# Performance work log

Hardware: AMD Instinct MI355X
Metric: run time of the kernel (lower is better)

## Reference

```python
import jax, jax.numpy as jnp
import numpy as np

B, S, D_MODEL = 4, 2048, 1024
NUM_HEADS, HEAD_DIM = 16, 64
EPS = 1e-6


def setup_inputs() -> dict:
    key = jax.random.key(0)
    ks = jax.random.split(key, 6)
    hd = NUM_HEADS * HEAD_DIM
    scale_in = 1.0 / np.sqrt(D_MODEL)
    scale_hd = 1.0 / np.sqrt(hd)
    return {
        "x": jax.random.normal(ks[0], (B, S, D_MODEL), dtype=jnp.float32),
        "w_q": jax.random.normal(ks[1], (D_MODEL, hd), dtype=jnp.float32) * scale_in,
        "w_k": jax.random.normal(ks[2], (D_MODEL, hd), dtype=jnp.float32) * scale_in,
        "w_v": jax.random.normal(ks[3], (D_MODEL, hd), dtype=jnp.float32) * scale_in,
        "w_proj": jax.random.normal(ks[4], (hd, D_MODEL), dtype=jnp.float32) * scale_hd,
        "b_proj": jax.random.normal(ks[5], (D_MODEL,), dtype=jnp.float32) * 0.01,
        "ln_gamma": jnp.ones((D_MODEL,), dtype=jnp.float32),
        "ln_beta": jnp.zeros((D_MODEL,), dtype=jnp.float32),
    }


def reference(x, w_q, w_k, w_v, w_proj, b_proj, ln_gamma, ln_beta):
    # x: [B, S, D]; project and split heads -> [B, H, S, Dh]
    def split_heads(t):
        b, s, _ = t.shape
        return t.reshape(b, s, NUM_HEADS, HEAD_DIM).transpose(0, 2, 1, 3)

    q = split_heads(x @ w_q)
    k = split_heads(x @ w_k)
    v = split_heads(x @ w_v)

    scale = HEAD_DIM ** (-0.5)
    attn = jnp.einsum("bnqd,bnkd->bnqk", q, k) * scale  # [B, H, S, S]
    attn = jax.nn.softmax(attn, axis=-1)
    o = jnp.einsum("bnqk,bnkd->bnqd", attn, v)  # [B, H, S, Dh]
    o = o.transpose(0, 2, 1, 3).reshape(x.shape[0], x.shape[1], NUM_HEADS * HEAD_DIM)

    # proj + residual (dropout = identity in eval) then LayerNorm(eps=1e-6)
    y = o @ w_proj + b_proj + x
    mean = jnp.mean(y, axis=-1, keepdims=True)
    var = jnp.var(y, axis=-1, keepdims=True)
    y = (y - mean) * jax.lax.rsqrt(var + EPS) * ln_gamma + ln_beta
    return y
```

## Files before the change

kernel.cpp:

```cpp
#include <hip/hip_runtime.h>
#include <hip/hip_fp16.h>


typedef unsigned short u16;
typedef __attribute__((ext_vector_type(8))) u16 u16x8;
typedef __attribute__((ext_vector_type(4))) u16 u16x4;
typedef __attribute__((ext_vector_type(2))) unsigned int u32x2;
typedef __attribute__((ext_vector_type(8))) __bf16 bf16x8;
typedef __attribute__((ext_vector_type(8))) _Float16 f16x8;
typedef __attribute__((ext_vector_type(4))) _Float16 f16x4;
typedef __attribute__((ext_vector_type(2))) _Float16 f16x2;
typedef __attribute__((ext_vector_type(2))) __fp16 hf16x2;
typedef __attribute__((ext_vector_type(4))) float f32x4;

#define SM_C1 0.1803368801111204f

static __device__ __forceinline__ u16 f2bf(float f) {
  union { float f; unsigned int u; } v; v.f = f;
  unsigned int u = v.u;
  return (u16)((u + 0x7fffu + ((u >> 16) & 1u)) >> 16);
}
static __device__ __forceinline__ float bf2f(u16 b) {
  union { unsigned int u; float f; } v; v.u = ((unsigned int)b) << 16;
  return v.f;
}
static __device__ __forceinline__ u16 f2h(float f) {
  union { _Float16 h; u16 u; } v; v.h = (_Float16)f;
  return v.u;
}

static __device__ __forceinline__ void gld16(const u16* g, u16* l) {
  __builtin_amdgcn_global_load_lds((const __attribute__((address_space(1))) void*)g,
                                   (__attribute__((address_space(3))) void*)l, 16, 0, 0);
}


__global__ __launch_bounds__(256) void k_convx(const float* __restrict__ x,
                                               u16* __restrict__ xbf) {
  int i = (blockIdx.x * 256 + threadIdx.x) * 8;
  float4 a = *(const float4*)(x + i);
  float4 b = *(const float4*)(x + i + 4);
  u16x8 o;
  o[0] = f2bf(a.x); o[1] = f2bf(a.y); o[2] = f2bf(a.z); o[3] = f2bf(a.w);
  o[4] = f2bf(b.x); o[5] = f2bf(b.y); o[6] = f2bf(b.z); o[7] = f2bf(b.w);
  *(u16x8*)(xbf + i) = o;
}

__global__ __launch_bounds__(256) void k_convwT(const float* __restrict__ w0,
                                                const float* __restrict__ w1,
                                                const float* __restrict__ w2,
                                                const float* __restrict__ w3,
                                                u16* __restrict__ o0, u16* __restrict__ o1,
                                                u16* __restrict__ o2, u16* __restrict__ o3) {
  __shared__ float tile[64][65];
  const float* w = blockIdx.z == 0 ? w0 : blockIdx.z == 1 ? w1 : blockIdx.z == 2 ? w2 : w3;
  u16* o = blockIdx.z == 0 ? o0 : blockIdx.z == 1 ? o1 : blockIdx.z == 2 ? o2 : o3;
  const int k0 = blockIdx.x * 64, n0 = blockIdx.y * 64;
  const int t = threadIdx.x;
#pragma unroll
  for (int i = 0; i < 16; i++) {
    int idx = t + 256 * i;
    int k = idx >> 6, n = idx & 63;
    tile[k][n] = w[(k0 + k) * 1024 + n0 + n];
  }
  __syncthreads();
#pragma unroll
  for (int i = 0; i < 16; i++) {
    int idx = t + 256 * i;
    int n = idx >> 6, k = idx & 63;
    o[(n0 + n) * 1024 + k0 + k] = f2bf(tile[k][n]);
  }
}


__global__ __launch_bounds__(256) void k_gemm_qkv(const u16* __restrict__ xbf,
                                                  const u16* __restrict__ wT,
                                                  u16* __restrict__ Qb, u16* __restrict__ Kb,
                                                  u16* __restrict__ VbT) {
  __shared__ alignas(16) u16 Als[128 * 64];
  __shared__ alignas(16) u16 Bls[128 * 64];
  const int t = threadIdx.x;
  const int wv = t >> 6, lane = t & 63, quad = lane >> 4, l16 = lane & 15;
  const int wm = wv >> 1, wn = wv & 1;
  const int m0 = blockIdx.x * 128;
  const int nt = blockIdx.y;
  const int row = t >> 3;
  const int kg = (t & 7) ^ (row & 7);
  const u16* aG = xbf + (size_t)(m0 + row) * 1024 + kg * 8;
  const u16* bG = wT + (size_t)(nt * 128 + row) * 1024 + kg * 8;
  const int sw = l16 & 7;
  const int aA0 = (wm * 64 + l16) * 64 + ((quad) ^ sw) * 8;
  const int aA1 = (wm * 64 + l16) * 64 + ((4 + quad) ^ sw) * 8;
  const int bA0 = (wn * 64 + l16) * 64 + ((quad) ^ sw) * 8;
  const int bA1 = (wn * 64 + l16) * 64 + ((4 + quad) ^ sw) * 8;

  f32x4 acc[4][4] = {};
  for (int k0 = 0; k0 < 1024; k0 += 64) {
    __syncthreads();
#pragma unroll
    for (int i = 0; i < 4; i++) {
      gld16(aG + i * 32 * 1024 + k0, &Als[(i * 256 + wv * 64) * 8]);
      gld16(bG + i * 32 * 1024 + k0, &Bls[(i * 256 + wv * 64) * 8]);
    }
    __syncthreads();
#pragma unroll
    for (int c = 0; c < 2; c++) {
      bf16x8 a[4], b[4];
#pragma unroll
      for (int f = 0; f < 4; f++) a[f] = *(const bf16x8*)&Als[(c ? aA1 : aA0) + f * 1024];
#pragma unroll
      for (int g = 0; g < 4; g++) b[g] = *(const bf16x8*)&Bls[(c ? bA1 : bA0) + g * 1024];
#pragma unroll
      for (int f = 0; f < 4; f++)
#pragma unroll
        for (int g = 0; g < 4; g++)
          acc[f][g] = __builtin_amdgcn_mfma_f32_16x16x32_bf16(a[f], b[g], acc[f][g], 0, 0, 0);
    }
  }

  const int sel = nt >> 3;
  const int n0 = (nt & 7) * 128 + wn * 64;
  const int mBase = m0 + wm * 64 + quad * 4;
  if (sel < 2) {
    u16* Ob = sel == 0 ? Qb : Kb;
    const float scl = sel == 0 ? SM_C1 : 1.0f;
#pragma unroll
    for (int f = 0; f < 4; f++)
#pragma unroll
      for (int g = 0; g < 4; g++)
#pragma unroll
        for (int r = 0; r < 4; r++) {
          int m = mBase + f * 16 + r;
          int n = n0 + g * 16 + l16;
          Ob[(size_t)m * 1024 + n] = f2bf(acc[f][g][r] * scl);
        }
  } else {
#pragma unroll
    for (int f = 0; f < 4; f++) {
      int m = mBase + f * 16;
      int bb = m >> 11, s = m & 2047;
#pragma unroll
      for (int g = 0; g < 4; g++) {
        int n = n0 + g * 16 + l16;
        int hh = n >> 6, dh = n & 63;
        u16x4 o;
#pragma unroll
        for (int r = 0; r < 4; r++) o[r] = f2h(acc[f][g][r]);
        *(u16x4*)&VbT[(size_t)(((bb << 4) + hh) * 64 + dh) * 2048 + s] = o;
      }
    }
  }
}


__global__ __launch_bounds__(256) void k_gemm_proj(const u16* __restrict__ Abf,
                                                   const u16* __restrict__ wT,
                                                   const float* __restrict__ x,
                                                   const float* __restrict__ bias,
                                                   u16* __restrict__ ypre) {
  __shared__ alignas(16) u16 Als[128 * 64];
  __shared__ alignas(16) u16 Bls[128 * 64];
  const int t = threadIdx.x;
  const int wv = t >> 6, lane = t & 63, quad = lane >> 4, l16 = lane & 15;
  const int wm = wv >> 1, wn = wv & 1;
  const int m0 = blockIdx.x * 128;
  const int n0t = blockIdx.y * 128;
  const int row = t >> 3;
  const int kg = (t & 7) ^ (row & 7);
  const u16* aG = Abf + (size_t)(m0 + row) * 1024 + kg * 8;
  const u16* bG = wT + (size_t)(n0t + row) * 1024 + kg * 8;
  const int sw = l16 & 7;
  const int aA0 = (wm * 64 + l16) * 64 + ((quad) ^ sw) * 8;
  const int aA1 = (wm * 64 + l16) * 64 + ((4 + quad) ^ sw) * 8;
  const int bA0 = (wn * 64 + l16) * 64 + ((quad) ^ sw) * 8;
  const int bA1 = (wn * 64 + l16) * 64 + ((4 + quad) ^ sw) * 8;

  f32x4 acc[4][4] = {};
  for (int k0 = 0; k0 < 1024; k0 += 64) {
    __syncthreads();
#pragma unroll
    for (int i = 0; i < 4; i++) {
      gld16(aG + i * 32 * 1024 + k0, &Als[(i * 256 + wv * 64) * 8]);
      gld16(bG + i * 32 * 1024 + k0, &Bls[(i * 256 + wv * 64) * 8]);
    }
    __syncthreads();
#pragma unroll
    for (int c = 0; c < 2; c++) {
      bf16x8 a[4], b[4];
#pragma unroll
      for (int f = 0; f < 4; f++) a[f] = *(const bf16x8*)&Als[(c ? aA1 : aA0) + f * 1024];
#pragma unroll
      for (int g = 0; g < 4; g++) b[g] = *(const bf16x8*)&Bls[(c ? bA1 : bA0) + g * 1024];
#pragma unroll
      for (int f = 0; f < 4; f++)
#pragma unroll
        for (int g = 0; g < 4; g++)
          acc[f][g] = __builtin_amdgcn_mfma_f32_16x16x32_bf16(a[f], b[g], acc[f][g], 0, 0, 0);
    }
  }

  const int n0 = n0t + wn * 64;
  const int mBase = m0 + wm * 64 + quad * 4;
#pragma unroll
  for (int g = 0; g < 4; g++) {
    int n = n0 + g * 16 + l16;
    float bn = bias[n];
#pragma unroll
    for (int f = 0; f < 4; f++)
#pragma unroll
      for (int r = 0; r < 4; r++) {
        int m = mBase + f * 16 + r;
        ypre[(size_t)m * 1024 + n] = f2bf(acc[f][g][r] + bn + x[(size_t)m * 1024 + n]);
      }
  }
}


__global__ __launch_bounds__(256, 2) void k_attn(const u16* __restrict__ Qb,
                                                 const u16* __restrict__ Kb,
                                                 const u16* __restrict__ VbT,
                                                 u16* __restrict__ Ob) {
  __shared__ alignas(16) u16 smem[4][64 * 72];
  const int b = blockIdx.x >> 4, h = blockIdx.x & 15;
  const int q0 = blockIdx.y * 256;
  const int t = threadIdx.x;
  const int wave = t >> 6, lane = t & 63, quad = lane >> 4, l16 = lane & 15;
  const int sr = t >> 2, sc = (t & 3) * 8;

  bf16x8 aq[4][2];
#pragma unroll
  for (int qf = 0; qf < 4; qf++)
#pragma unroll
    for (int c = 0; c < 2; c++)
      aq[qf][c] = *(const bf16x8*)&Qb[(size_t)(b * 2048 + q0 + wave * 64 + qf * 16 + l16) * 1024 +
                                      h * 64 + c * 32 + quad * 8];

  f32x4 Oacc[4][4] = {};
  float psum[4] = {};

  const u16* kBase = Kb + (size_t)(b * 2048) * 1024 + h * 64;
  const u16* vtRow = VbT + (size_t)((b * 16 + h) * 64 + sr) * 2048;

  u16x8 rk0, rk1, rv0, rv1;
  {
    const u16* kR = kBase + (size_t)sr * 1024;
    rk0 = *(const u16x8*)(kR + sc);
    rk1 = *(const u16x8*)(kR + sc + 32);
    rv0 = *(const u16x8*)(vtRow + sc);
    rv1 = *(const u16x8*)(vtRow + sc + 32);
  }

  for (int kt = 0; kt < 32; kt++) {
    const int p = kt & 1;
    u16* Kls = smem[p];
    u16* Vls = smem[2 + p];
    *(u16x8*)&Kls[sr * 72 + sc]      = rk0;
    *(u16x8*)&Kls[sr * 72 + sc + 32] = rk1;
    *(u16x8*)&Vls[sr * 72 + sc]      = rv0;
    *(u16x8*)&Vls[sr * 72 + sc + 32] = rv1;
    __syncthreads();
    if (kt < 31) {
      const int kv1 = (kt + 1) * 64;
      const u16* kR = kBase + (size_t)(kv1 + sr) * 1024;
      rk0 = *(const u16x8*)(kR + sc);
      rk1 = *(const u16x8*)(kR + sc + 32);
      rv0 = *(const u16x8*)(vtRow + kv1 + sc);
      rv1 = *(const u16x8*)(vtRow + kv1 + sc + 32);
    }

    f32x4 st[4][4];
#pragma unroll
    for (int qf = 0; qf < 4; qf++)
#pragma unroll
      for (int f = 0; f < 4; f++) st[qf][f] = f32x4{0.f, 0.f, 0.f, 0.f};
#pragma unroll
    for (int c = 0; c < 2; c++) {
      bf16x8 bk[4];
#pragma unroll
      for (int f = 0; f < 4; f++)
        bk[f] = *(const bf16x8*)&Kls[(f * 16 + l16) * 72 + c * 32 + quad * 8];
#pragma unroll
      for (int qf = 0; qf < 4; qf++)
#pragma unroll
        for (int f = 0; f < 4; f++)
          st[qf][f] = __builtin_amdgcn_mfma_f32_16x16x32_bf16(bk[f], aq[qf][c], st[qf][f], 0, 0, 0);
    }

    f16x8 va[2][4];
#pragma unroll
    for (int kf = 0; kf < 2; kf++)
#pragma unroll
      for (int g = 0; g < 4; g++)
        va[kf][g] = *(const f16x8*)&Vls[(g * 16 + l16) * 72 + kf * 32 + quad * 8];

#pragma unroll
    for (int qf = 0; qf < 4; qf++) {
      union PK { hf16x2 r; f16x2 v; __half2 h; unsigned int u; };
      PK e01[4], e23[4];
      __half2 it2 = __half2{__half(0.f), __half(0.f)};
#pragma unroll
      for (int f = 0; f < 4; f++) {
        PK a01, a23;
        a01.r = __builtin_amdgcn_cvt_pkrtz(st[qf][f][0], st[qf][f][1]);
        a23.r = __builtin_amdgcn_cvt_pkrtz(st[qf][f][2], st[qf][f][3]);
        e01[f].h = h2exp2(a01.h);
        e23[f].h = h2exp2(a23.h);
        it2 = __hadd2(it2, __hadd2(e01[f].h, e23[f].h));
      }
      psum[qf] += __low2float(it2) + __high2float(it2);
#pragma unroll
      for (int kf = 0; kf < 2; kf++) {
        u32x2 sa = __builtin_amdgcn_permlane32_swap(e01[2 * kf].u, e01[2 * kf + 1].u, false, false);
        u32x2 sb = __builtin_amdgcn_permlane32_swap(e23[2 * kf].u, e23[2 * kf + 1].u, false, false);
        u32x2 ta = __builtin_amdgcn_permlane16_swap(sa[0], sa[1], false, false);
        u32x2 tb = __builtin_amdgcn_permlane16_swap(sb[0], sb[1], false, false);
        union { unsigned int u[4]; f16x8 v; } pb;
        pb.u[0] = ta[0];
        pb.u[1] = tb[0];
        pb.u[2] = ta[1];
        pb.u[3] = tb[1];
#pragma unroll
        for (int g = 0; g < 4; g++)
          Oacc[qf][g] = __builtin_amdgcn_mfma_f32_16x16x32_f16(va[kf][g], pb.v, Oacc[qf][g], 0, 0, 0);
      }
    }
  }

  float inv[4];
#pragma unroll
  for (int qf = 0; qf < 4; qf++) {
    float v = psum[qf];
    v += __shfl_xor(v, 16);
    v += __shfl_xor(v, 32);
    inv[qf] = 1.f / v;
  }

  __syncthreads();
  u16* Ols = (u16*)smem;
#pragma unroll
  for (int qf = 0; qf < 4; qf++)
#pragma unroll
    for (int g = 0; g < 4; g++) {
      u16x4 o;
#pragma unroll
      for (int r = 0; r < 4; r++) o[r] = f2bf(Oacc[qf][g][r] * inv[qf]);
      *(u16x4*)&Ols[(wave * 64 + qf * 16 + l16) * 72 + g * 16 + quad * 4] = o;
    }
  __syncthreads();
  u16* gO = Ob + (size_t)(b * 2048 + q0 + t) * 1024 + h * 64;
#pragma unroll
  for (int j = 0; j < 8; j++)
    *(u16x8*)(gO + j * 8) = *(const u16x8*)&Ols[t * 72 + j * 8];
}


__global__ __launch_bounds__(256) void k_ln(const u16* __restrict__ y,
                                            const float* __restrict__ g,
                                            const float* __restrict__ bt,
                                            float* __restrict__ out) {
  const int row = blockIdx.x;
  const int t = threadIdx.x;
  u16x4 rv = *(const u16x4*)(y + row * 1024 + t * 4);
  float vx = bf2f(rv[0]), vy = bf2f(rv[1]), vz = bf2f(rv[2]), vw = bf2f(rv[3]);
  float s1 = vx + vy + vz + vw;
  float s2 = vx * vx + vy * vy + vz * vz + vw * vw;
#pragma unroll
  for (int off = 32; off; off >>= 1) {
    s1 += __shfl_down(s1, off);
    s2 += __shfl_down(s2, off);
  }
  __shared__ float red[10];
  const int wave = t >> 6, lane = t & 63;
  if (lane == 0) { red[wave] = s1; red[4 + wave] = s2; }
  __syncthreads();
  if (t == 0) {
    float a = red[0] + red[1] + red[2] + red[3];
    float bsum = red[4] + red[5] + red[6] + red[7];
    float mean = a * (1.f / 1024.f);
    float var = bsum * (1.f / 1024.f) - mean * mean;
    red[8] = mean;
    red[9] = rsqrtf(var + 1e-6f);
  }
  __syncthreads();
  float mean = red[8], iv = red[9];
  float4 gv = *(const float4*)(g + t * 4);
  float4 bv = *(const float4*)(bt + t * 4);
  float4 o;
  o.x = (vx - mean) * iv * gv.x + bv.x;
  o.y = (vy - mean) * iv * gv.y + bv.y;
  o.z = (vz - mean) * iv * gv.z + bv.z;
  o.w = (vw - mean) * iv * gv.w + bv.w;
  *(float4*)(out + row * 1024 + t * 4) = o;
}


extern "C" void kernel_launch(void* const* d_in, const int* in_sizes, int n_in,
                              void* d_out, int out_size, void* d_ws, size_t ws_size,
                              hipStream_t stream) {
  const float* x  = (const float*)d_in[0];
  const float* wq = (const float*)d_in[1];
  const float* wk = (const float*)d_in[2];
  const float* wv = (const float*)d_in[3];
  const float* wp = (const float*)d_in[4];
  const float* bp = (const float*)d_in[5];
  const float* g  = (const float*)d_in[6];
  const float* bt = (const float*)d_in[7];
  float* out = (float*)d_out;
  char* ws = (char*)d_ws;

  u16* xbf = (u16*)(ws);
  u16* wqT = (u16*)(ws + (16 << 20));
  u16* wkT = wqT + (size_t)1024 * 1024;
  u16* wvT = wqT + (size_t)2048 * 1024;
  u16* wpT = (u16*)(ws + (22 << 20));
  u16* Qb  = (u16*)(ws + (24 << 20));
  u16* Kb  = (u16*)(ws + (40 << 20));
  u16* VbT = (u16*)(ws + (56 << 20));
  u16* Ob  = (u16*)(ws);
  u16* ypre = (u16*)(ws + (24 << 20));

  k_convx<<<4096, 256, 0, stream>>>(x, xbf);
  k_convwT<<<dim3(16, 16, 4), 256, 0, stream>>>(wq, wk, wv, wp, wqT, wkT, wvT, wpT);
  k_gemm_qkv<<<dim3(64, 24), 256, 0, stream>>>(xbf, wqT, Qb, Kb, VbT);
  k_attn<<<dim3(64, 8), 256, 0, stream>>>(Qb, Kb, VbT, Ob);
  k_gemm_proj<<<dim3(64, 8), 256, 0, stream>>>(Ob, wpT, x, bp, ypre);
  k_ln<<<8192, 256, 0, stream>>>(ypre, g, bt, out);
}
```

Baseline: 270.7 us.

## Rewrite QKV GEMM as 256x256 double-buffered 8-wave pipeline with priority hints

The QKV projection GEMM moves from 128x128 tiles with 4 waves and single-buffered LDS to 256x256 tiles with 8 waves and double-buffered LDS. The next K tile is prefetched with global_load_lds while the current one is computed, and LDS fragment reads are interleaved with MFMA clusters separated by barriers. s_setprio hints are added around MFMA blocks in both the GEMM and the attention kernel, aiming to overlap memory with compute and raise per-block reuse. The cost is much larger LDS (128KB per block) and more accumulator registers, with only 384 blocks in the grid, which may hurt occupancy and tail balance.

Result: slower. 288.3 us (+6.5%).

```diff
diff --git a/kernel.cpp b/kernel.cpp
--- a/kernel.cpp
+++ b/kernel.cpp
@@ -33,6 +33,10 @@
   __builtin_amdgcn_global_load_lds((const __attribute__((address_space(1))) void*)g,
                                    (__attribute__((address_space(3))) void*)l, 16, 0, 0);
 }
+
+#define QBAR() do { asm volatile("" ::: "memory"); __builtin_amdgcn_s_barrier(); \
+                    __builtin_amdgcn_sched_barrier(0); } while (0)
+#define QDRAIN() asm volatile("s_waitcnt vmcnt(0)" ::: "memory")
 
 
 __global__ __launch_bounds__(256) void k_convx(const float* __restrict__ x,
@@ -73,75 +77,143 @@
 }
 
 
-__global__ __launch_bounds__(256) void k_gemm_qkv(const u16* __restrict__ xbf,
-                                                  const u16* __restrict__ wT,
-                                                  u16* __restrict__ Qb, u16* __restrict__ Kb,
-                                                  u16* __restrict__ VbT) {
-  __shared__ alignas(16) u16 Als[128 * 64];
-  __shared__ alignas(16) u16 Bls[128 * 64];
+__global__ __launch_bounds__(512, 2) void k_gemm_qkv(const u16* __restrict__ xbf,
+                                                     const u16* __restrict__ wT,
+                                                     u16* __restrict__ Qb, u16* __restrict__ Kb,
+                                                     u16* __restrict__ VbT) {
+  __shared__ alignas(16) u16 As[2][256 * 64];
+  __shared__ alignas(16) u16 Bs[2][256 * 64];
   const int t = threadIdx.x;
   const int wv = t >> 6, lane = t & 63, quad = lane >> 4, l16 = lane & 15;
-  const int wm = wv >> 1, wn = wv & 1;
-  const int m0 = blockIdx.x * 128;
+  const int wm = wv >> 2, wn = wv & 3;
+  const int m0 = blockIdx.x * 256;
   const int nt = blockIdx.y;
-  const int row = t >> 3;
-  const int kg = (t & 7) ^ (row & 7);
-  const u16* aG = xbf + (size_t)(m0 + row) * 1024 + kg * 8;
-  const u16* bG = wT + (size_t)(nt * 128 + row) * 1024 + kg * 8;
+  const int srow = t >> 3;
+  const int kg = (t & 7) ^ (srow & 7);
+  const u16* aG = xbf + (size_t)(m0 + srow) * 1024 + kg * 8;
+  const u16* bG = wT + (size_t)(nt * 256 + srow) * 1024 + kg * 8;
   const int sw = l16 & 7;
-  const int aA0 = (wm * 64 + l16) * 64 + ((quad) ^ sw) * 8;
-  const int aA1 = (wm * 64 + l16) * 64 + ((4 + quad) ^ sw) * 8;
-  const int bA0 = (wn * 64 + l16) * 64 + ((quad) ^ sw) * 8;
-  const int bA1 = (wn * 64 + l16) * 64 + ((4 + quad) ^ sw) * 8;
-
-  f32x4 acc[4][4] = {};
-  for (int k0 = 0; k0 < 1024; k0 += 64) {
-    __syncthreads();
-#pragma unroll
-    for (int i = 0; i < 4; i++) {
-      gld16(aG + i * 32 * 1024 + k0, &Als[(i * 256 + wv * 64) * 8]);
-      gld16(bG + i * 32 * 1024 + k0, &Bls[(i * 256 + wv * 64) * 8]);
-    }
-    __syncthreads();
-#pragma unroll
-    for (int c = 0; c < 2; c++) {
-      bf16x8 a[4], b[4];
-#pragma unroll
-      for (int f = 0; f < 4; f++) a[f] = *(const bf16x8*)&Als[(c ? aA1 : aA0) + f * 1024];
-#pragma unroll
-      for (int g = 0; g < 4; g++) b[g] = *(const bf16x8*)&Bls[(c ? bA1 : bA0) + g * 1024];
-#pragma unroll
-      for (int f = 0; f < 4; f++)
-#pragma unroll
-        for (int g = 0; g < 4; g++)
-          acc[f][g] = __builtin_amdgcn_mfma_f32_16x16x32_bf16(a[f], b[g], acc[f][g], 0, 0, 0);
-    }
-  }
-
-  const int sel = nt >> 3;
-  const int n0 = (nt & 7) * 128 + wn * 64;
-  const int mBase = m0 + wm * 64 + quad * 4;
+  const int ldsDst = (wv * 64) * 8;
+
+  f32x4 acc[8][4] = {};
+
+  auto STAGE = [&](int tl) {
+    const int q_ = tl & 1;
+    const int k0_ = tl * 64;
+#pragma unroll
+    for (int i = 0; i < 4; i++)
+      gld16(aG + i * 64 * 1024 + k0_, &As[q_][i * 4096 + ldsDst]);
+#pragma unroll
+    for (int i = 0; i < 4; i++)
+      gld16(bG + i * 64 * 1024 + k0_, &Bs[q_][i * 4096 + ldsDst]);
+  };
+
+  STAGE(0);
+  QDRAIN();
+  QBAR();
+
+  for (int tile = 0; tile < 16; ++tile) {
+    const int p = tile & 1;
+    bf16x8 a[4][2], b[4][2];
+
+#pragma unroll
+    for (int j = 0; j < 4; j++)
+#pragma unroll
+      for (int kk = 0; kk < 2; kk++)
+        a[j][kk] = *(const bf16x8*)&As[p][(wm * 128 + j * 16 + l16) * 64 +
+                                          ((kk * 4 + quad) ^ sw) * 8];
+#pragma unroll
+    for (int j = 0; j < 2; j++)
+#pragma unroll
+      for (int kk = 0; kk < 2; kk++)
+        b[j][kk] = *(const bf16x8*)&Bs[p][(wn * 64 + j * 16 + l16) * 64 +
+                                          ((kk * 4 + quad) ^ sw) * 8];
+    if (tile < 15) STAGE(tile + 1);
+    QBAR();
+    __builtin_amdgcn_s_setprio(1);
+#pragma unroll
+    for (int j = 0; j < 4; j++)
+#pragma unroll
+      for (int n = 0; n < 2; n++)
+#pragma unroll
+        for (int kk = 0; kk < 2; kk++)
+          acc[j][n] = __builtin_amdgcn_mfma_f32_16x16x32_bf16(a[j][kk], b[n][kk], acc[j][n], 0, 0, 0);
+    __builtin_amdgcn_s_setprio(0);
+    QBAR();
+
+#pragma unroll
+    for (int j = 0; j < 2; j++)
+#pragma unroll
+      for (int kk = 0; kk < 2; kk++)
+        b[2 + j][kk] = *(const bf16x8*)&Bs[p][(wn * 64 + (2 + j) * 16 + l16) * 64 +
+                                              ((kk * 4 + quad) ^ sw) * 8];
+    QBAR();
+    __builtin_amdgcn_s_setprio(1);
+#pragma unroll
+    for (int j = 0; j < 4; j++)
+#pragma unroll
+      for (int n = 0; n < 2; n++)
+#pragma unroll
+        for (int kk = 0; kk < 2; kk++)
+          acc[j][2 + n] = __builtin_amdgcn_mfma_f32_16x16x32_bf16(a[j][kk], b[2 + n][kk], acc[j][2 + n], 0, 0, 0);
+    __builtin_amdgcn_s_setprio(0);
+    QBAR();
+
+#pragma unroll
+    for (int j = 0; j < 4; j++)
+#pragma unroll
+      for (int kk = 0; kk < 2; kk++)
+        a[j][kk] = *(const bf16x8*)&As[p][(wm * 128 + 64 + j * 16 + l16) * 64 +
+                                          ((kk * 4 + quad) ^ sw) * 8];
+    QBAR();
+    __builtin_amdgcn_s_setprio(1);
+#pragma unroll
+    for (int j = 0; j < 4; j++)
+#pragma unroll
+      for (int n = 0; n < 2; n++)
+#pragma unroll
+        for (int kk = 0; kk < 2; kk++)
+          acc[4 + j][2 + n] = __builtin_amdgcn_mfma_f32_16x16x32_bf16(a[j][kk], b[2 + n][kk], acc[4 + j][2 + n], 0, 0, 0);
+    __builtin_amdgcn_s_setprio(0);
+    QBAR();
+
+    __builtin_amdgcn_s_setprio(1);
+#pragma unroll
+    for (int j = 0; j < 4; j++)
+#pragma unroll
+      for (int n = 0; n < 2; n++)
+#pragma unroll
+        for (int kk = 0; kk < 2; kk++)
+          acc[4 + j][n] = __builtin_amdgcn_mfma_f32_16x16x32_bf16(a[j][kk], b[n][kk], acc[4 + j][n], 0, 0, 0);
+    __builtin_amdgcn_s_setprio(0);
+    QDRAIN();
+    QBAR();
+  }
+
+  const int sel = nt >> 2;
+  const int nin = (nt & 3) * 256 + wn * 64;
+  const int mBase = m0 + wm * 128 + quad * 4;
   if (sel < 2) {
     u16* Ob = sel == 0 ? Qb : Kb;
     const float scl = sel == 0 ? SM_C1 : 1.0f;
 #pragma unroll
-    for (int f = 0; f < 4; f++)
+    for (int f = 0; f < 8; f++)
 #pragma unroll
       for (int g = 0; g < 4; g++)
 #pragma unroll
         for (int r = 0; r < 4; r++) {
           int m = mBase + f * 16 + r;
-          int n = n0 + g * 16 + l16;
+          int n = nin + g * 16 + l16;
           Ob[(size_t)m * 1024 + n] = f2bf(acc[f][g][r] * scl);
         }
   } else {
 #pragma unroll
-    for (int f = 0; f < 4; f++) {
+    for (int f = 0; f < 8; f++) {
       int m = mBase + f * 16;
       int bb = m >> 11, s = m & 2047;
 #pragma unroll
       for (int g = 0; g < 4; g++) {
-        int n = n0 + g * 16 + l16;
+        int n = nin + g * 16 + l16;
         int hh = n >> 6, dh = n & 63;
         u16x4 o;
 #pragma unroll
@@ -273,6 +345,7 @@
     for (int qf = 0; qf < 4; qf++)
 #pragma unroll
       for (int f = 0; f < 4; f++) st[qf][f] = f32x4{0.f, 0.f, 0.f, 0.f};
+    __builtin_amdgcn_s_setprio(1);
 #pragma unroll
     for (int c = 0; c < 2; c++) {
       bf16x8 bk[4];
@@ -285,6 +358,7 @@
         for (int f = 0; f < 4; f++)
           st[qf][f] = __builtin_amdgcn_mfma_f32_16x16x32_bf16(bk[f], aq[qf][c], st[qf][f], 0, 0, 0);
     }
+    __builtin_amdgcn_s_setprio(0);
 
     f16x8 va[2][4];
 #pragma unroll
@@ -308,6 +382,7 @@
         it2 = __hadd2(it2, __hadd2(e01[f].h, e23[f].h));
       }
       psum[qf] += __low2float(it2) + __high2float(it2);
+      __builtin_amdgcn_s_setprio(1);
 #pragma unroll
       for (int kf = 0; kf < 2; kf++) {
         u32x2 sa = __builtin_amdgcn_permlane32_swap(e01[2 * kf].u, e01[2 * kf + 1].u, false, false);
@@ -323,6 +398,7 @@
         for (int g = 0; g < 4; g++)
           Oacc[qf][g] = __builtin_amdgcn_mfma_f32_16x16x32_f16(va[kf][g], pb.v, Oacc[qf][g], 0, 0, 0);
       }
+      __builtin_amdgcn_s_setprio(0);
     }
   }
 
@@ -421,7 +497,7 @@
 
   k_convx<<<4096, 256, 0, stream>>>(x, xbf);
   k_convwT<<<dim3(16, 16, 4), 256, 0, stream>>>(wq, wk, wv, wp, wqT, wkT, wvT, wpT);
-  k_gemm_qkv<<<dim3(64, 24), 256, 0, stream>>>(xbf, wqT, Qb, Kb, VbT);
+  k_gemm_qkv<<<dim3(32, 12), 512, 0, stream>>>(xbf, wqT, Qb, Kb, VbT);
   k_attn<<<dim3(64, 8), 256, 0, stream>>>(Qb, Kb, VbT, Ob);
   k_gemm_proj<<<dim3(64, 8), 256, 0, stream>>>(Ob, wpT, x, bp, ypre);
   k_ln<<<8192, 256, 0, stream>>>(ypre, g, bt, out);
```

## Stage K/V tiles via direct global-to-LDS loads with XOR-swizzled layout

Applied to the files above, without the earlier changes.

The attention kernel now stages K and V^T tiles with global_load_lds (direct to LDS) instead of loading into registers and writing to shared memory. The padded 72-wide rows become an unpadded 64-wide layout with an XOR swizzle to avoid bank conflicts. The barrier moves to the end of each iteration after a vmcnt drain, so the next tile's loads overlap the current compute. This cuts VGPR pressure and LDS store instructions, but the per-iteration full vmcnt drain may expose some load latency.

New measurement: 267.0 us, median of 2. About the same (-1.4%).

```diff
diff --git a/kernel.cpp b/kernel.cpp
--- a/kernel.cpp
+++ b/kernel.cpp
@@ -33,6 +33,10 @@
   __builtin_amdgcn_global_load_lds((const __attribute__((address_space(1))) void*)g,
                                    (__attribute__((address_space(3))) void*)l, 16, 0, 0);
 }
+
+#define QBAR() do { asm volatile("" ::: "memory"); __builtin_amdgcn_s_barrier(); \
+                    asm volatile("" ::: "memory"); } while (0)
+#define QDRAIN() asm volatile("s_waitcnt vmcnt(0)" ::: "memory")
 
 
 __global__ __launch_bounds__(256) void k_convx(const float* __restrict__ x,
@@ -225,7 +229,7 @@
   const int q0 = blockIdx.y * 256;
   const int t = threadIdx.x;
   const int wave = t >> 6, lane = t & 63, quad = lane >> 4, l16 = lane & 15;
-  const int sr = t >> 2, sc = (t & 3) * 8;
+  const int sw = l16 & 7;
 
   bf16x8 aq[4][2];
 #pragma unroll
@@ -239,34 +243,30 @@
   float psum[4] = {};
 
   const u16* kBase = Kb + (size_t)(b * 2048) * 1024 + h * 64;
-  const u16* vtRow = VbT + (size_t)((b * 16 + h) * 64 + sr) * 2048;
-
-  u16x8 rk0, rk1, rv0, rv1;
-  {
-    const u16* kR = kBase + (size_t)sr * 1024;
-    rk0 = *(const u16x8*)(kR + sc);
-    rk1 = *(const u16x8*)(kR + sc + 32);
-    rv0 = *(const u16x8*)(vtRow + sc);
-    rv1 = *(const u16x8*)(vtRow + sc + 32);
-  }
+  const u16* vBase = VbT + (size_t)((b * 16 + h) * 64) * 2048;
+
+  const int sRow0 = t >> 3, sG0 = (t & 7) ^ (sRow0 & 7);
+  const int sRow1 = (256 + t) >> 3, sG1 = (t & 7) ^ (sRow1 & 7);
+
+  auto STAGE = [&](int kt, int p) {
+    const int kv = kt * 64;
+    u16* Kls = smem[p];
+    u16* Vls = smem[2 + p];
+    gld16(kBase + (size_t)(kv + sRow0) * 1024 + sG0 * 8, &Kls[(wave * 64) * 8]);
+    gld16(kBase + (size_t)(kv + sRow1) * 1024 + sG1 * 8, &Kls[(256 + wave * 64) * 8]);
+    gld16(vBase + (size_t)sRow0 * 2048 + kv + sG0 * 8, &Vls[(wave * 64) * 8]);
+    gld16(vBase + (size_t)sRow1 * 2048 + kv + sG1 * 8, &Vls[(256 + wave * 64) * 8]);
+  };
+
+  STAGE(0, 0);
+  QDRAIN();
+  QBAR();
 
   for (int kt = 0; kt < 32; kt++) {
     const int p = kt & 1;
     u16* Kls = smem[p];
     u16* Vls = smem[2 + p];
-    *(u16x8*)&Kls[sr * 72 + sc]      = rk0;
-    *(u16x8*)&Kls[sr * 72 + sc + 32] = rk1;
-    *(u16x8*)&Vls[sr * 72 + sc]      = rv0;
-    *(u16x8*)&Vls[sr * 72 + sc + 32] = rv1;
-    __syncthreads();
-    if (kt < 31) {
-      const int kv1 = (kt + 1) * 64;
-      const u16* kR = kBase + (size_t)(kv1 + sr) * 1024;
-      rk0 = *(const u16x8*)(kR + sc);
-      rk1 = *(const u16x8*)(kR + sc + 32);
-      rv0 = *(const u16x8*)(vtRow + kv1 + sc);
-      rv1 = *(const u16x8*)(vtRow + kv1 + sc + 32);
-    }
+    if (kt < 31) STAGE(kt + 1, p ^ 1);
 
     f32x4 st[4][4];
 #pragma unroll
@@ -278,7 +278,7 @@
       bf16x8 bk[4];
 #pragma unroll
       for (int f = 0; f < 4; f++)
-        bk[f] = *(const bf16x8*)&Kls[(f * 16 + l16) * 72 + c * 32 + quad * 8];
+        bk[f] = *(const bf16x8*)&Kls[(f * 16 + l16) * 64 + ((c * 4 + quad) ^ sw) * 8];
 #pragma unroll
       for (int qf = 0; qf < 4; qf++)
 #pragma unroll
@@ -291,7 +291,7 @@
     for (int kf = 0; kf < 2; kf++)
 #pragma unroll
       for (int g = 0; g < 4; g++)
-        va[kf][g] = *(const f16x8*)&Vls[(g * 16 + l16) * 72 + kf * 32 + quad * 8];
+        va[kf][g] = *(const f16x8*)&Vls[(g * 16 + l16) * 64 + ((kf * 4 + quad) ^ sw) * 8];
 
 #pragma unroll
     for (int qf = 0; qf < 4; qf++) {
@@ -324,6 +324,9 @@
           Oacc[qf][g] = __builtin_amdgcn_mfma_f32_16x16x32_f16(va[kf][g], pb.v, Oacc[qf][g], 0, 0, 0);
       }
     }
+
+    QDRAIN();
+    QBAR();
   }
 
   float inv[4];
@@ -335,7 +338,6 @@
     inv[qf] = 1.f / v;
   }
 
-  __syncthreads();
   u16* Ols = (u16*)smem;
 #pragma unroll
   for (int qf = 0; qf < 4; qf++)
```
